# Kernel tuning notes

Hardware: AMD Instinct MI355X
Metric: run time of the kernel (lower is better)

## Reference

```python
import jax, jax.numpy as jnp
import numpy as np

BETA_MIN = 1e-06
GAMMA_INIT = 0.1
NUM_FEATURES = 256
BATCH = 262144

def setup_inputs() -> dict:
    key = jax.random.key(0)
    kx, = jax.random.split(key, 1)
    x = jax.random.normal(kx, (BATCH, NUM_FEATURES), dtype=jnp.float32)
    beta = jnp.ones((NUM_FEATURES,), dtype=jnp.float32)
    gamma = jnp.eye(NUM_FEATURES, dtype=jnp.float32) * GAMMA_INIT
    return {"x": x, "beta": beta, "gamma": gamma}

def reference(x, beta, gamma):
    # GDN (non-inverse): y = x / sqrt((x^2) @ gamma + max(beta, beta_min))
    beta_c = jnp.maximum(beta, jnp.asarray(BETA_MIN, dtype=beta.dtype))
    norm_pool = jnp.einsum('bi,ij->bj', x * x, gamma) + beta_c  # [B, F]
    norm_pool = jnp.sqrt(norm_pool)
    return x / norm_pool
```

## Files before the change

### kernel.cpp

```cpp
#include <hip/hip_runtime.h>
#include <hip/hip_bf16.h>

#define FEAT   256
#define TROWS  16
#define TBYTES (TROWS * FEAT * 4)

typedef __attribute__((ext_vector_type(8))) short  short8;
typedef __attribute__((ext_vector_type(4))) float  floatx4;

__device__ __forceinline__ short f2bf(float f) {
    __hip_bfloat16 h = __float2bfloat16(f);
    return __builtin_bit_cast(short, h);
}

__device__ __forceinline__ unsigned swz(unsigned o) {
    return o ^ (((o >> 10) & 7u) << 4);
}

__global__ __launch_bounds__(256, 2) void gdn_kernel(
    const float* __restrict__ x,
    const float* __restrict__ beta,
    const float* __restrict__ gamma,
    float* __restrict__ out,
    int batch)
{
    __shared__ char ldsx[2 * TBYTES];

    const int tid  = threadIdx.x;
    const int lane = tid & 63;
    const int wave = tid >> 6;
    const int l15  = lane & 15;
    const int grp  = lane >> 4;
    const int colbase = wave * 64;

    short8 Bf[4][8];
    #pragma unroll
    for (int nt = 0; nt < 4; ++nt) {
        const int col = colbase + nt * 16 + l15;
        #pragma unroll
        for (int ks = 0; ks < 8; ++ks) {
            const int k0 = ks * 32 + grp * 8;
            short8 b;
            #pragma unroll
            for (int i = 0; i < 8; ++i)
                b[i] = f2bf(gamma[(size_t)(k0 + i) * FEAT + col]);
            Bf[nt][ks] = b;
        }
    }

    float bc[4];
    #pragma unroll
    for (int nt = 0; nt < 4; ++nt)
        bc[nt] = fmaxf(beta[colbase + nt * 16 + l15], 1e-6f);

    const int ntiles = batch >> 4;
    const int stride = gridDim.x;

    auto STAGE = [&](int buf, int t) {
        const char* gb = (const char*)x + (size_t)t * TBYTES;
        #pragma unroll
        for (int r = 0; r < 4; ++r) {
            const unsigned d = (unsigned)(tid * 16 + r * 4096);
            __builtin_amdgcn_global_load_lds(
                (const __attribute__((address_space(1))) void*)(gb + swz(d)),
                (__attribute__((address_space(3))) void*)(&ldsx[buf * TBYTES] + d),
                16, 0, 0);
        }
    };

    int cur = 0;
    STAGE(0, blockIdx.x);
    __syncthreads();

    for (int t = blockIdx.x; t < ntiles; t += stride) {
        const int tn = t + stride;
        if (tn < ntiles) STAGE(cur ^ 1, tn);

        const char* lb = &ldsx[cur * TBYTES];

        const unsigned p0 = (unsigned)(l15 * 1024 + grp * 32);
        const unsigned xv = (unsigned)((l15 & 7) << 4);
        short8 Af[8];
        #pragma unroll
        for (int ks = 0; ks < 8; ++ks) {
            floatx4 v0 = *(const floatx4*)(lb + (((p0 + ks * 128))      ^ xv));
            floatx4 v1 = *(const floatx4*)(lb + (((p0 + ks * 128 + 16)) ^ xv));
            short8 a;
            #pragma unroll
            for (int i = 0; i < 4; ++i) {
                a[i]     = f2bf(v0[i] * v0[i]);
                a[4 + i] = f2bf(v1[i] * v1[i]);
            }
            Af[ks] = a;
        }

        floatx4 acc[4] = {{0.f,0.f,0.f,0.f},{0.f,0.f,0.f,0.f},
                          {0.f,0.f,0.f,0.f},{0.f,0.f,0.f,0.f}};
        #pragma unroll
        for (int ks = 0; ks < 8; ++ks) {
            #pragma unroll
            for (int nt = 0; nt < 4; ++nt) {
                acc[nt] = __builtin_amdgcn_mfma_f32_16x16x32_bf16(
                    Af[ks], Bf[nt][ks], acc[nt], 0, 0, 0);
            }
        }

        const int rb = t << 4;
        #pragma unroll
        for (int nt = 0; nt < 4; ++nt) {
            const int col = colbase + nt * 16 + l15;
            #pragma unroll
            for (int r = 0; r < 4; ++r) {
                const int row = grp * 4 + r;
                const unsigned eo = (unsigned)(row * 1024 + col * 4);
                const float xval = *(const float*)(lb + (eo ^ (((unsigned)(row & 7)) << 4)));
                out[(size_t)(rb + row) * FEAT + col] = xval * rsqrtf(acc[nt][r] + bc[nt]);
            }
        }

        __syncthreads();
        cur ^= 1;
    }
}

extern "C" void kernel_launch(void* const* d_in, const int* in_sizes, int n_in,
                              void* d_out, int out_size, void* d_ws, size_t ws_size,
                              hipStream_t stream) {
    const float* x     = (const float*)d_in[0];
    const float* beta  = (const float*)d_in[1];
    const float* gamma = (const float*)d_in[2];
    float* out = (float*)d_out;

    const int batch = in_sizes[0] / FEAT;

    dim3 grid(512);
    dim3 block(256);
    hipLaunchKernelGGL(gdn_kernel, grid, block, 0, stream,
                       x, beta, gamma, out, batch);
}
```

Measured before the change: 115.7 us.

## Triple-buffer x tiles with prefetch distance two and explicit vmcnt waits

Moves the LDS staging of x from double to triple buffering. Each block now keeps two tile loads in flight, and the blocking __syncthreads is replaced by raw s_barrier plus a partial s_waitcnt vmcnt so only the current tile's loads must complete. The aim is to hide more global-load latency in this bandwidth-bound kernel. In exchange it uses more LDS per block, issues redundant clamped loads at the tail, and assumes the tile count divides evenly by the grid. The vmcnt threshold also counts outstanding stores, so it may wait longer than needed.

```diff
diff --git a/kernel.cpp b/kernel.cpp
--- a/kernel.cpp
+++ b/kernel.cpp
@@ -4,6 +4,7 @@
 #define FEAT   256
 #define TROWS  16
 #define TBYTES (TROWS * FEAT * 4)
+#define NBUF   3
 
 typedef __attribute__((ext_vector_type(8))) short  short8;
 typedef __attribute__((ext_vector_type(4))) float  floatx4;
@@ -24,7 +25,7 @@
     float* __restrict__ out,
     int batch)
 {
-    __shared__ char ldsx[2 * TBYTES];
+    __shared__ char ldsx[NBUF * TBYTES];
 
     const int tid  = threadIdx.x;
     const int lane = tid & 63;
@@ -55,36 +56,47 @@
 
     const int ntiles = batch >> 4;
     const int stride = gridDim.x;
+    const int iters  = ntiles / stride;
+    const int t0     = blockIdx.x;
 
-    auto STAGE = [&](int buf, int t) {
+    auto STAGE = [&](int s, int t) {
         const char* gb = (const char*)x + (size_t)t * TBYTES;
+        char* lbase = &ldsx[s * TBYTES];
         #pragma unroll
         for (int r = 0; r < 4; ++r) {
             const unsigned d = (unsigned)(tid * 16 + r * 4096);
             __builtin_amdgcn_global_load_lds(
                 (const __attribute__((address_space(1))) void*)(gb + swz(d)),
-                (__attribute__((address_space(3))) void*)(&ldsx[buf * TBYTES] + d),
+                (__attribute__((address_space(3))) void*)(lbase + d),
                 16, 0, 0);
         }
     };
 
-    int cur = 0;
-    STAGE(0, blockIdx.x);
-    __syncthreads();
+    STAGE(0, t0);
+    STAGE(1, t0 + stride);
 
-    for (int t = blockIdx.x; t < ntiles; t += stride) {
-        const int tn = t + stride;
-        if (tn < ntiles) STAGE(cur ^ 1, tn);
+    for (int it = 0; it < iters; ++it) {
+        __builtin_amdgcn_s_barrier();
+        __builtin_amdgcn_sched_barrier(0);
 
-        const char* lb = &ldsx[cur * TBYTES];
+        int itn = it + 2;
+        if (itn >= iters) itn = iters - 1;
+        STAGE((it + 2) % NBUF, t0 + itn * stride);
+
+        asm volatile("s_waitcnt vmcnt(8)" ::: "memory");
+        __builtin_amdgcn_sched_barrier(0);
+        __builtin_amdgcn_s_barrier();
+        __builtin_amdgcn_sched_barrier(0);
+
+        const char* lb = &ldsx[(it % NBUF) * TBYTES];
 
         const unsigned p0 = (unsigned)(l15 * 1024 + grp * 32);
         const unsigned xv = (unsigned)((l15 & 7) << 4);
         short8 Af[8];
         #pragma unroll
         for (int ks = 0; ks < 8; ++ks) {
-            floatx4 v0 = *(const floatx4*)(lb + (((p0 + ks * 128))      ^ xv));
-            floatx4 v1 = *(const floatx4*)(lb + (((p0 + ks * 128 + 16)) ^ xv));
+            floatx4 v0 = *(const floatx4*)(lb + ((p0 + ks * 128)      ^ xv));
+            floatx4 v1 = *(const floatx4*)(lb + ((p0 + ks * 128 + 16) ^ xv));
             short8 a;
             #pragma unroll
             for (int i = 0; i < 4; ++i) {
@@ -105,7 +117,7 @@
             }
         }
 
-        const int rb = t << 4;
+        const int rb = (t0 + it * stride) << 4;
         #pragma unroll
         for (int nt = 0; nt < 4; ++nt) {
             const int col = colbase + nt * 16 + l15;
@@ -117,9 +129,6 @@
                 out[(size_t)(rb + row) * FEAT + col] = xval * rsqrtf(acc[nt][r] + bc[nt]);
             }
         }
-
-        __syncthreads();
-        cur ^= 1;
     }
 }
 
```

Result: faster. 108.4 us (-6.3%).
